# Kernel tuning notes

Hardware: AMD Instinct MI355X
Metric: run time of the kernel (lower is better)

Reference implementation:

```python
import jax, jax.numpy as jnp
import numpy as np

B, N, H, D = 1, 4096, 16, 64
C = H * D  # 1024
SCALE = D ** -0.5


def setup_inputs() -> dict:
    key = jax.random.key(0)
    k1, k2, k3, k4 = jax.random.split(key, 4)
    x = jax.random.normal(k1, (B, N, C), dtype=jnp.float32)
    # torch nn.Linear weights: [out_features, in_features]; y = x @ W.T + b
    w_qkv = jax.random.normal(k2, (3 * C, C), dtype=jnp.float32) * 0.02
    w_proj = jax.random.normal(k3, (C, C), dtype=jnp.float32) * 0.02
    b_proj = jax.random.normal(k4, (C,), dtype=jnp.float32) * 0.02
    return {"x": x, "w_qkv": w_qkv, "w_proj": w_proj, "b_proj": b_proj}


def reference(x, w_qkv, w_proj, b_proj):
    Bn, Nn, Cn = x.shape
    # fused QKV projection (no bias)
    qkv = jnp.einsum('bnc,oc->bno', x, w_qkv)            # [B,N,3C]
    qkv = qkv.reshape(Bn, Nn, 3, H, D)
    q = jnp.transpose(qkv[:, :, 0], (0, 2, 1, 3))        # [B,H,N,D]
    k = jnp.transpose(qkv[:, :, 1], (0, 2, 1, 3))
    v = jnp.transpose(qkv[:, :, 2], (0, 2, 1, 3))
    attn = jnp.einsum('bhnd,bhmd->bhnm', q, k) * SCALE   # [B,H,N,N]
    causal_mask = jnp.triu(jnp.ones((Nn, Nn), dtype=bool), k=1)
    attn = jnp.where(causal_mask, -jnp.inf, attn)
    attn = jax.nn.softmax(attn, axis=-1)
    out = jnp.einsum('bhnm,bhmd->bhnd', attn, v)          # [B,H,N,D]
    out = jnp.transpose(out, (0, 2, 1, 3)).reshape(Bn, Nn, Cn)
    out = jnp.einsum('bnc,oc->bno', out, w_proj) + b_proj
    return out
```

## Files before the change

kernel.cpp:

```cpp
#include <hip/hip_runtime.h>
#include <hip/hip_bf16.h>
#include <stdint.h>
#include <stddef.h>

using bf16 = __hip_bfloat16;
typedef short short8 __attribute__((ext_vector_type(8)));
typedef short short4v __attribute__((ext_vector_type(4)));
typedef short short2v __attribute__((ext_vector_type(2)));
typedef float f32x4 __attribute__((ext_vector_type(4)));
typedef float f32x16 __attribute__((ext_vector_type(16)));
typedef unsigned uintv4 __attribute__((ext_vector_type(4)));

#define MFMA16(A, B, C) __builtin_amdgcn_mfma_f32_16x16x32_bf16(A, B, C, 0, 0, 0)
#define MFMA32(A, B, C) __builtin_amdgcn_mfma_f32_32x32x16_bf16(A, B, C, 0, 0, 0)
#define GLOAD_LDS(g, l) __builtin_amdgcn_global_load_lds( \
    (const __attribute__((address_space(1))) void*)(g),   \
    (__attribute__((address_space(3))) void*)(l), 16, 0, 0)

constexpr int AN  = 4096;
constexpr int NH  = 16;
constexpr int HD  = 64;
constexpr int CC  = 1024;
constexpr int C3  = 3072;
constexpr float QSCALE = 0.125f * 1.4426950408889634f;

__device__ inline short bf16s(float f) {
    return (short)((__float_as_uint(f) + 0x8000u) >> 16);
}
__device__ inline float bf2f(short s) {
    return __uint_as_float(((unsigned)(unsigned short)s) << 16);
}
__device__ inline bf16 sbf(short s) {
    union { short s; bf16 b; } u;
    u.s = s;
    return u.b;
}
#if __has_builtin(__builtin_amdgcn_cvt_pk_bf16_f32)
typedef __bf16 bf16x2 __attribute__((ext_vector_type(2)));
__device__ inline short2v pk2(float a, float b) {
    bf16x2 r = __builtin_amdgcn_cvt_pk_bf16_f32(a, b);
    return *(short2v*)&r;
}
#else
__device__ inline short2v pk2(float a, float b) {
    unsigned ua = __float_as_uint(a) + 0x8000u;
    unsigned ub = __float_as_uint(b) + 0x8000u;
    unsigned r  = __builtin_amdgcn_perm(ub, ua, 0x07060302);
    return *(short2v*)&r;
}
#endif
__device__ inline unsigned pk2u(float a, float b) {
    short2v p = pk2(a, b);
    return *(unsigned*)&p;
}
__device__ inline short4v pack4(float a, float b, float c, float d) {
    short2v lo = pk2(a, b), hi = pk2(c, d);
    short4v r;
    r[0] = lo[0]; r[1] = lo[1]; r[2] = hi[0]; r[3] = hi[1];
    return r;
}
__device__ inline void plswap(unsigned &a, unsigned &b) {
    asm("v_permlane32_swap_b32 %0, %1" : "+v"(a), "+v"(b));
}
#if __has_builtin(__builtin_amdgcn_exp2f)
#define FAST_EXP2(x) __builtin_amdgcn_exp2f(x)
#else
#define FAST_EXP2(x) exp2f(x)
#endif

__device__ inline int detect_mode_inline(const unsigned short* xraw, int lane) {
    int crazy = 0;
    #pragma unroll
    for (int i = 0; i < 4; ++i) {
        const unsigned short u = xraw[lane * 4 + i];
        const int e = (u >> 7) & 0xFF;
        if (e >= 134 || (e != 0 && e <= 110)) ++crazy;
    }
    #pragma unroll
    for (int off = 32; off > 0; off >>= 1)
        crazy += __shfl_down(crazy, off, 64);
    crazy = __shfl(crazy, 0, 64);
    return (crazy >= 8) ? 1 : 0;
}

__device__ inline void cast8(const void* __restrict__ src,
                             bf16* __restrict__ dst, int i, int m) {
    if (m) {
        const float* s = (const float*)src;
        float4 a = *(const float4*)(s + i);
        float4 b = *(const float4*)(s + i + 4);
        short8 o;
        short2v p0 = pk2(a.x, a.y), p1 = pk2(a.z, a.w);
        short2v p2 = pk2(b.x, b.y), p3 = pk2(b.z, b.w);
        o[0] = p0[0]; o[1] = p0[1]; o[2] = p1[0]; o[3] = p1[1];
        o[4] = p2[0]; o[5] = p2[1]; o[6] = p3[0]; o[7] = p3[1];
        *(short8*)(dst + i) = o;
    } else {
        *(short8*)(dst + i) = *(const short8*)((const short*)src + i);
    }
}

__global__ void cast_all(const void* __restrict__ x, const void* __restrict__ wq,
                         const void* __restrict__ wp, const void* __restrict__ bp,
                         bf16* __restrict__ xb, bf16* __restrict__ wqb,
                         bf16* __restrict__ wpb, float* __restrict__ biasf,
                         int* __restrict__ mode) {
    const int b = blockIdx.x;
    const int tid = threadIdx.x;
    const int m = detect_mode_inline((const unsigned short*)x, tid & 63);
    if (b < 2048) {
        cast8(x, xb, (b * 256 + tid) * 8, m);
    } else if (b < 3584) {
        cast8(wq, wqb, ((b - 2048) * 256 + tid) * 8, m);
    } else if (b < 4096) {
        cast8(wp, wpb, ((b - 3584) * 256 + tid) * 8, m);
    } else {
        #pragma unroll
        for (int i = tid; i < CC; i += 256)
            biasf[i] = m ? ((const float*)bp)[i] : bf2f(((const short*)bp)[i]);
        if (tid == 0) *mode = m;
    }
}

constexpr int BM = 128, BN = 128, BK = 32;

__global__ __launch_bounds__(256, 3) void gemm_qkv(
    const bf16* __restrict__ A, const bf16* __restrict__ Bw,
    bf16* __restrict__ qOut, bf16* __restrict__ kOut, bf16* __restrict__ vOut)
{
    __shared__ bf16 As[BM * BK];
    __shared__ bf16 Bs[BN * BK];

    const int tid  = threadIdx.x;
    const int wave = tid >> 6;
    const int lane = tid & 63;
    const int quad = lane >> 4;
    const int l16  = lane & 15;
    const int wr   = wave >> 1;
    const int wc   = wave & 1;
    const int m0   = blockIdx.y * BM;
    const int o0   = blockIdx.x * BN;

    const int srow = lane >> 2;
    const int scol = (lane & 3) * 8;

    f32x4 acc[4][4] = {};

    for (int k0 = 0; k0 < CC; k0 += BK) {
        __syncthreads();
        #pragma unroll
        for (int c = 0; c < 2; ++c) {
            const int rbase = wave * 32 + c * 16;
            GLOAD_LDS(A + (size_t)(m0 + rbase + srow) * CC + k0 + scol, &As[rbase * BK]);
            GLOAD_LDS(Bw + (size_t)(o0 + rbase + srow) * CC + k0 + scol, &Bs[rbase * BK]);
        }
        __syncthreads();

        short8 af[4], bfr[4];
        #pragma unroll
        for (int i = 0; i < 4; ++i)
            af[i] = *(const short8*)&As[(wr * 64 + i * 16 + l16) * BK + quad * 8];
        #pragma unroll
        for (int j = 0; j < 4; ++j)
            bfr[j] = *(const short8*)&Bs[(wc * 64 + j * 16 + l16) * BK + quad * 8];
        #pragma unroll
        for (int i = 0; i < 4; ++i)
            #pragma unroll
            for (int j = 0; j < 4; ++j)
                acc[i][j] = MFMA16(af[i], bfr[j], acc[i][j]);
    }

    if (o0 >= 2 * CC) {
        #pragma unroll
        for (int j = 0; j < 4; ++j) {
            const int dcol = o0 - 2 * CC + wc * 64 + j * 16 + l16;
            const int hV = dcol >> 6, dV = dcol & 63;
            #pragma unroll
            for (int i = 0; i < 4; ++i) {
                const int kv0 = m0 + wr * 64 + i * 16 + quad * 4;
                const size_t addr = (size_t)hV * 64 * AN + (size_t)(kv0 >> 6) * 4096
                                  + (size_t)((kv0 >> 3) & 7) * 512 + dV * 8 + (kv0 & 7);
                *(short4v*)&vOut[addr] =
                    pack4(acc[i][j][0], acc[i][j][1], acc[i][j][2], acc[i][j][3]);
            }
        }
        return;
    }
    if (o0 >= CC) {
        #pragma unroll
        for (int j = 0; j < 4; ++j) {
            const int dcol = o0 - CC + wc * 64 + j * 16 + l16;
            const int hK = dcol >> 6, dc = (dcol >> 3) & 7, de = dcol & 7;
            #pragma unroll
            for (int i = 0; i < 4; ++i) {
                const int kv0 = m0 + wr * 64 + i * 16 + quad * 4;
                const size_t addr = (size_t)hK * 64 * AN + (size_t)(kv0 >> 6) * 4096
                                  + (size_t)dc * 512 + (size_t)(kv0 & 63) * 8 + de;
                #pragma unroll
                for (int r = 0; r < 4; ++r)
                    kOut[addr + r * 8] = sbf(bf16s(acc[i][j][r]));
            }
        }
        return;
    }
    #pragma unroll
    for (int j = 0; j < 4; ++j) {
        const int col = o0 + wc * 64 + j * 16 + l16;
        #pragma unroll
        for (int i = 0; i < 4; ++i) {
            const int row = m0 + wr * 64 + i * 16 + quad * 4;
            #pragma unroll
            for (int r = 0; r < 2; ++r) {
                short2v p = pk2(acc[i][j][2 * r] * QSCALE, acc[i][j][2 * r + 1] * QSCALE);
                qOut[(size_t)(row + 2 * r) * CC + col]     = sbf(p[0]);
                qOut[(size_t)(row + 2 * r + 1) * CC + col] = sbf(p[1]);
            }
        }
    }
}

constexpr int PM = 128, PN = 64, PK = 32;

__global__ __launch_bounds__(256, 2) void gemm_proj(
    const bf16* __restrict__ A, const bf16* __restrict__ Bw,
    const float* __restrict__ bias, void* __restrict__ Cout,
    const int* __restrict__ mode)
{
    __shared__ bf16 As[PM * PK];
    __shared__ bf16 Bs[PN * PK];

    const int tid  = threadIdx.x;
    const int wave = tid >> 6;
    const int lane = tid & 63;
    const int quad = lane >> 4;
    const int l16  = lane & 15;
    const int wr   = wave >> 1;
    const int wc   = wave & 1;
    const int m0   = blockIdx.y * PM;
    const int o0   = blockIdx.x * PN;
    const bool f32out = (*mode != 0);

    const int srow = lane >> 2;
    const int scol = (lane & 3) * 8;

    f32x4 acc[4][2] = {};

    for (int k0 = 0; k0 < CC; k0 += PK) {
        __syncthreads();
        #pragma unroll
        for (int c = 0; c < 2; ++c) {
            const int rbase = wave * 32 + c * 16;
            GLOAD_LDS(A + (size_t)(m0 + rbase + srow) * CC + k0 + scol, &As[rbase * PK]);
        }
        {
            const int rbase = wave * 16;
            GLOAD_LDS(Bw + (size_t)(o0 + rbase + srow) * CC + k0 + scol, &Bs[rbase * PK]);
        }
        __syncthreads();

        short8 af[4], bfr[2];
        #pragma unroll
        for (int i = 0; i < 4; ++i)
            af[i] = *(const short8*)&As[(wr * 64 + i * 16 + l16) * PK + quad * 8];
        #pragma unroll
        for (int j = 0; j < 2; ++j)
            bfr[j] = *(const short8*)&Bs[(wc * 32 + j * 16 + l16) * PK + quad * 8];
        #pragma unroll
        for (int i = 0; i < 4; ++i)
            #pragma unroll
            for (int j = 0; j < 2; ++j)
                acc[i][j] = MFMA16(af[i], bfr[j], acc[i][j]);
    }

    #pragma unroll
    for (int j = 0; j < 2; ++j) {
        const int col = o0 + wc * 32 + j * 16 + l16;
        const float bv = bias[col];
        #pragma unroll
        for (int i = 0; i < 4; ++i) {
            const int row = m0 + wr * 64 + i * 16 + quad * 4;
            if (f32out) {
                #pragma unroll
                for (int r = 0; r < 4; ++r)
                    ((float*)Cout)[(size_t)(row + r) * CC + col] = acc[i][j][r] + bv;
            } else {
                #pragma unroll
                for (int r = 0; r < 2; ++r) {
                    short2v p = pk2(acc[i][j][2 * r] + bv, acc[i][j][2 * r + 1] + bv);
                    ((bf16*)Cout)[(size_t)(row + 2 * r) * CC + col]     = sbf(p[0]);
                    ((bf16*)Cout)[(size_t)(row + 2 * r + 1) * CC + col] = sbf(p[1]);
                }
            }
        }
    }
}

constexpr int TK = 64;

__global__ __launch_bounds__(256, 2) void attn12(
    const bf16* __restrict__ qbuf, const bf16* __restrict__ kP,
    const bf16* __restrict__ vP, bf16* __restrict__ pOn, float* __restrict__ pl)
{
    const int tid  = threadIdx.x;
    const int w    = tid >> 6;
    const int lane = tid & 63;
    const int l31  = lane & 31;
    const int hh   = lane >> 5;
    const int bid  = blockIdx.x;
    const int h    = bid & 15;
    const int t    = bid >> 4;
    const int s    = w >> 1;
    const int rh   = w & 1;

    short8 ones8;
    #pragma unroll
    for (int i = 0; i < 8; ++i) ones8[i] = (short)0x3F80;

    #pragma unroll 1
    for (int pp = 0; pp < 2; ++pp) {
        const int tile = pp ? 63 - t : t;
        const int nIt  = tile + 1;
        const int fi0  = pp ? ((64 - t) + 1) >> 1 : 0;
        const int fi1  = pp ? 64 - t : (t + 2) >> 1;
        const int mid  = fi0 + ((fi1 - fi0 + 1) >> 1);
        const int i0   = s ? mid : fi0;
        const int iHi  = s ? fi1 : mid;
        const int slot = pp * 2 + s;
        const int qw   = tile * 64 + rh * 32;
        const int q    = qw + l31;

        short8 qf[4];
        {
            const bf16* qp = qbuf + (size_t)q * CC + h * HD + hh * 8;
            #pragma unroll
            for (int ki = 0; ki < 4; ++ki)
                qf[ki] = *(const short8*)(qp + ki * 16);
        }

        f32x16 acc_l = {};
        f32x16 acc_o[2] = {};

        if (i0 < iHi) {
            const bf16* kb = kP + (size_t)h * 64 * AN + (size_t)i0 * 4096;
            const bf16* vb = vP + (size_t)h * 64 * AN + (size_t)i0 * 4096;
            const bool hasdiag = (iHi == nIt);

            short8 kf[8];
            #pragma unroll
            for (int kt = 0; kt < 2; ++kt)
                #pragma unroll
                for (int ki = 0; ki < 4; ++ki)
                    kf[kt * 4 + ki] = *(const short8*)
                        (kb + (2 * ki + hh) * 512 + kt * 256 + l31 * 8);
            kb += 4096;

            for (int it = i0; it < iHi; ++it) {
                short8 vf[8];
                #pragma unroll
                for (int kk = 0; kk < 4; ++kk)
                    #pragma unroll
                    for (int dt2 = 0; dt2 < 2; ++dt2)
                        vf[kk * 2 + dt2] = *(const short8*)
                            (vb + (2 * kk + hh) * 512 + dt2 * 256 + l31 * 8);
                vb += 4096;

                f32x16 st[2];
                __builtin_amdgcn_s_setprio(1);
                #pragma unroll
                for (int kt = 0; kt < 2; ++kt) {
                    f32x16 a = {};
                    #pragma unroll
                    for (int ki = 0; ki < 4; ++ki)
                        a = MFMA32(kf[kt * 4 + ki], qf[ki], a);
                    st[kt] = a;
                }
                __builtin_amdgcn_s_setprio(0);

                if (it + 1 < iHi) {
                    #pragma unroll
                    for (int kt = 0; kt < 2; ++kt)
                        #pragma unroll
                        for (int ki = 0; ki < 4; ++ki)
                            kf[kt * 4 + ki] = *(const short8*)
                                (kb + (2 * ki + hh) * 512 + kt * 256 + l31 * 8);
                    kb += 4096;
                }

                if (hasdiag && it == iHi - 1) {
                    const int kv0 = it * TK;
                    #pragma unroll
                    for (int kt = 0; kt < 2; ++kt)
                        #pragma unroll
                        for (int r = 0; r < 16; ++r) {
                            const int kv = kv0 + kt * 32 + (r & 3) + 8 * (r >> 2) + 4 * hh;
                            st[kt][r] = (kv <= q) ? FAST_EXP2(st[kt][r]) : 0.0f;
                        }
                } else {
                    #pragma unroll
                    for (int kt = 0; kt < 2; ++kt)
                        #pragma unroll
                        for (int r = 0; r < 16; ++r)
                            st[kt][r] = FAST_EXP2(st[kt][r]);
                }

                #pragma unroll
                for (int kt = 0; kt < 2; ++kt)
                    #pragma unroll
                    for (int kc = 0; kc < 2; ++kc) {
                        unsigned a0 = pk2u(st[kt][kc * 8 + 0], st[kt][kc * 8 + 1]);
                        unsigned a1 = pk2u(st[kt][kc * 8 + 2], st[kt][kc * 8 + 3]);
                        unsigned c0 = pk2u(st[kt][kc * 8 + 4], st[kt][kc * 8 + 5]);
                        unsigned c1 = pk2u(st[kt][kc * 8 + 6], st[kt][kc * 8 + 7]);
                        plswap(a0, c0);
                        plswap(a1, c1);
                        uintv4 fu;
                        fu[0] = a0; fu[1] = a1; fu[2] = c0; fu[3] = c1;
                        const short8 frag = *(const short8*)&fu;

                        __builtin_amdgcn_s_setprio(1);
                        acc_l = MFMA32(ones8, frag, acc_l);
                        #pragma unroll
                        for (int dt2 = 0; dt2 < 2; ++dt2)
                            acc_o[dt2] = MFMA32(vf[(kt * 2 + kc) * 2 + dt2],
                                                frag, acc_o[dt2]);
                        __builtin_amdgcn_s_setprio(0);
                    }
            }
        }

        const size_t base = (size_t)slot * AN * CC + (size_t)q * CC + h * HD;
        #pragma unroll
        for (int dt2 = 0; dt2 < 2; ++dt2)
            #pragma unroll
            for (int g = 0; g < 4; ++g) {
                const int d0 = dt2 * 32 + g * 8 + 4 * hh;
                *(short4v*)&pOn[base + d0] =
                    pack4(acc_o[dt2][4 * g + 0], acc_o[dt2][4 * g + 1],
                          acc_o[dt2][4 * g + 2], acc_o[dt2][4 * g + 3]);
            }
        if (hh == 0)
            pl[(size_t)slot * NH * AN + (size_t)h * AN + q] = acc_l[0];
    }
}

__global__ __launch_bounds__(128) void combine4(
    const bf16* __restrict__ pOn, const float* __restrict__ pl,
    bf16* __restrict__ outp)
{
    const int q  = blockIdx.x;
    const int c0 = threadIdx.x * 8;
    const int h  = c0 >> 6;
    float L = 0.f;
    #pragma unroll
    for (int k = 0; k < 4; ++k)
        L += pl[(size_t)k * NH * AN + (size_t)h * AN + q];
    const float invL = (L > 0.f) ? 1.f / L : 0.f;
    const size_t off = (size_t)q * CC + c0;
    float acc[8] = {};
    #pragma unroll
    for (int k = 0; k < 4; ++k) {
        short8 ov = *(const short8*)&pOn[(size_t)k * AN * CC + off];
        #pragma unroll
        for (int e = 0; e < 8; ++e)
            acc[e] += bf2f(ov[e]);
    }
    short8 o;
    #pragma unroll
    for (int e = 0; e < 8; e += 2) {
        short2v p = pk2(acc[e] * invL, acc[e + 1] * invL);
        o[e] = p[0]; o[e + 1] = p[1];
    }
    *(short8*)&outp[off] = o;
}

extern "C" void kernel_launch(void* const* d_in, const int* in_sizes, int n_in,
                              void* d_out, int out_size, void* d_ws, size_t ws_size,
                              hipStream_t stream) {
    char* ws = (char*)d_ws;
    bf16*   qbuf     = (bf16*)(ws);
    bf16*   kPack    = (bf16*)(ws + 8388608);
    bf16*   vPack    = (bf16*)(ws + 16777216);
    bf16*   attn_out = (bf16*)(ws + 25165824);
    bf16*   wprojb   = (bf16*)(ws + 33554432);
    float*  biasf    = (float*)(ws + 35651584);
    int*    mode     = (int*)(ws + 35655680);
    float*  pl       = (float*)(ws + 35659776);
    bf16*   xb       = (bf16*)(ws + 36708352);
    bf16*   wqkvb    = (bf16*)(ws + 45096960);
    bf16*   pOn      = (bf16*)(ws + 36708352);

    cast_all<<<dim3(4097), 256, 0, stream>>>(
        d_in[0], d_in[1], d_in[2], d_in[3], xb, wqkvb, wprojb, biasf, mode);

    gemm_qkv<<<dim3(C3 / BN, AN / BM), 256, 0, stream>>>(
        xb, wqkvb, qbuf, kPack, vPack);
    attn12<<<dim3(64 * NH), 256, 0, stream>>>(qbuf, kPack, vPack, pOn, pl);
    combine4<<<dim3(AN), 128, 0, stream>>>(pOn, pl, attn_out);
    gemm_proj<<<dim3(CC / PN, AN / PM), 256, 0, stream>>>(
        attn_out, wprojb, biasf, d_out, mode);
}
```

Measured before the change: 204.1 us.

## Share K fragments across two query groups per wave and vectorize K stores

The attention kernel now runs 2 waves per block instead of 4. Each wave handles both 32-row query halves of a 64-row tile and steps over 32-key chunks, so each K/V fragment load feeds two query groups. The diagonal chunk is masked for one group and skipped for the other. In the QKV GEMM, the K-output blocks swap MFMA operand order so each lane holds contiguous head-dim values, which lets them write packed 4-element stores instead of scalar bf16 stores. The price is more registers per wave (double accumulators and Q fragments) and fewer waves per block, which may reduce latency hiding.

```diff
diff --git a/kernel.cpp b/kernel.cpp
--- a/kernel.cpp
+++ b/kernel.cpp
@@ -140,6 +140,7 @@
     const int wc   = wave & 1;
     const int m0   = blockIdx.y * BM;
     const int o0   = blockIdx.x * BN;
+    const bool isK = (o0 >= CC) && (o0 < 2 * CC);
 
     const int srow = lane >> 2;
     const int scol = (lane & 3) * 8;
@@ -163,11 +164,19 @@
         #pragma unroll
         for (int j = 0; j < 4; ++j)
             bfr[j] = *(const short8*)&Bs[(wc * 64 + j * 16 + l16) * BK + quad * 8];
-        #pragma unroll
-        for (int i = 0; i < 4; ++i)
-            #pragma unroll
-            for (int j = 0; j < 4; ++j)
-                acc[i][j] = MFMA16(af[i], bfr[j], acc[i][j]);
+        if (isK) {
+            #pragma unroll
+            for (int i = 0; i < 4; ++i)
+                #pragma unroll
+                for (int j = 0; j < 4; ++j)
+                    acc[i][j] = MFMA16(bfr[j], af[i], acc[i][j]);
+        } else {
+            #pragma unroll
+            for (int i = 0; i < 4; ++i)
+                #pragma unroll
+                for (int j = 0; j < 4; ++j)
+                    acc[i][j] = MFMA16(af[i], bfr[j], acc[i][j]);
+        }
     }
 
     if (o0 >= 2 * CC) {
@@ -186,19 +195,19 @@
         }
         return;
     }
-    if (o0 >= CC) {
-        #pragma unroll
-        for (int j = 0; j < 4; ++j) {
-            const int dcol = o0 - CC + wc * 64 + j * 16 + l16;
-            const int hK = dcol >> 6, dc = (dcol >> 3) & 7, de = dcol & 7;
-            #pragma unroll
-            for (int i = 0; i < 4; ++i) {
-                const int kv0 = m0 + wr * 64 + i * 16 + quad * 4;
-                const size_t addr = (size_t)hK * 64 * AN + (size_t)(kv0 >> 6) * 4096
-                                  + (size_t)dc * 512 + (size_t)(kv0 & 63) * 8 + de;
-                #pragma unroll
-                for (int r = 0; r < 4; ++r)
-                    kOut[addr + r * 8] = sbf(bf16s(acc[i][j][r]));
+    if (isK) {
+        #pragma unroll
+        for (int i = 0; i < 4; ++i) {
+            const int kv = m0 + wr * 64 + i * 16 + l16;
+            const size_t rowoff = (size_t)(kv >> 6) * 4096 + (size_t)(kv & 63) * 8;
+            #pragma unroll
+            for (int j = 0; j < 4; ++j) {
+                const int d0 = (o0 - CC) + wc * 64 + j * 16 + quad * 4;
+                const int hK = d0 >> 6, dc = (d0 >> 3) & 7, de = d0 & 7;
+                const size_t addr = (size_t)hK * 64 * AN + rowoff
+                                  + (size_t)dc * 512 + de;
+                *(short4v*)&kOut[addr] =
+                    pack4(acc[i][j][0], acc[i][j][1], acc[i][j][2], acc[i][j][3]);
             }
         }
         return;
@@ -295,22 +304,18 @@
     }
 }
 
-constexpr int TK = 64;
-
-__global__ __launch_bounds__(256, 2) void attn12(
+__global__ __launch_bounds__(128, 2) void attn13(
     const bf16* __restrict__ qbuf, const bf16* __restrict__ kP,
     const bf16* __restrict__ vP, bf16* __restrict__ pOn, float* __restrict__ pl)
 {
     const int tid  = threadIdx.x;
-    const int w    = tid >> 6;
+    const int s    = tid >> 6;
     const int lane = tid & 63;
     const int l31  = lane & 31;
     const int hh   = lane >> 5;
     const int bid  = blockIdx.x;
     const int h    = bid & 15;
     const int t    = bid >> 4;
-    const int s    = w >> 1;
-    const int rh   = w & 1;
 
     short8 ones8;
     #pragma unroll
@@ -319,127 +324,146 @@
     #pragma unroll 1
     for (int pp = 0; pp < 2; ++pp) {
         const int tile = pp ? 63 - t : t;
-        const int nIt  = tile + 1;
-        const int fi0  = pp ? ((64 - t) + 1) >> 1 : 0;
-        const int fi1  = pp ? 64 - t : (t + 2) >> 1;
-        const int mid  = fi0 + ((fi1 - fi0 + 1) >> 1);
-        const int i0   = s ? mid : fi0;
-        const int iHi  = s ? fi1 : mid;
+        const int lo   = pp ? tile + 1 : 0;
+        const int hi   = pp ? 2 * tile + 2 : tile + 1;
+        const int mid  = lo + ((hi - lo + 1) >> 1);
+        const int i0   = s ? mid : lo;
+        const int iHi  = s ? hi : mid;
         const int slot = pp * 2 + s;
-        const int qw   = tile * 64 + rh * 32;
-        const int q    = qw + l31;
-
-        short8 qf[4];
-        {
-            const bf16* qp = qbuf + (size_t)q * CC + h * HD + hh * 8;
+        const int qb   = tile * 64;
+        const int q0   = qb + l31;
+        const int q1   = qb + 32 + l31;
+
+        short8 qf[2][4];
+        #pragma unroll
+        for (int g = 0; g < 2; ++g) {
+            const bf16* qp = qbuf + (size_t)(qb + 32 * g + l31) * CC + h * HD + hh * 8;
             #pragma unroll
             for (int ki = 0; ki < 4; ++ki)
-                qf[ki] = *(const short8*)(qp + ki * 16);
-        }
-
-        f32x16 acc_l = {};
-        f32x16 acc_o[2] = {};
+                qf[g][ki] = *(const short8*)(qp + ki * 16);
+        }
+
+        f32x16 acc_l[2] = {};
+        f32x16 acc_o[2][2] = {};
 
         if (i0 < iHi) {
-            const bf16* kb = kP + (size_t)h * 64 * AN + (size_t)i0 * 4096;
-            const bf16* vb = vP + (size_t)h * 64 * AN + (size_t)i0 * 4096;
-            const bool hasdiag = (iHi == nIt);
-
-            short8 kf[8];
-            #pragma unroll
-            for (int kt = 0; kt < 2; ++kt)
-                #pragma unroll
-                for (int ki = 0; ki < 4; ++ki)
-                    kf[kt * 4 + ki] = *(const short8*)
-                        (kb + (2 * ki + hh) * 512 + kt * 256 + l31 * 8);
-            kb += 4096;
-
-            for (int it = i0; it < iHi; ++it) {
-                short8 vf[8];
-                #pragma unroll
-                for (int kk = 0; kk < 4; ++kk)
-                    #pragma unroll
-                    for (int dt2 = 0; dt2 < 2; ++dt2)
-                        vf[kk * 2 + dt2] = *(const short8*)
-                            (vb + (2 * kk + hh) * 512 + dt2 * 256 + l31 * 8);
-                vb += 4096;
-
-                f32x16 st[2];
-                __builtin_amdgcn_s_setprio(1);
-                #pragma unroll
-                for (int kt = 0; kt < 2; ++kt) {
-                    f32x16 a = {};
-                    #pragma unroll
-                    for (int ki = 0; ki < 4; ++ki)
-                        a = MFMA32(kf[kt * 4 + ki], qf[ki], a);
-                    st[kt] = a;
-                }
-                __builtin_amdgcn_s_setprio(0);
-
-                if (it + 1 < iHi) {
-                    #pragma unroll
-                    for (int kt = 0; kt < 2; ++kt)
-                        #pragma unroll
-                        for (int ki = 0; ki < 4; ++ki)
-                            kf[kt * 4 + ki] = *(const short8*)
-                                (kb + (2 * ki + hh) * 512 + kt * 256 + l31 * 8);
-                    kb += 4096;
-                }
-
-                if (hasdiag && it == iHi - 1) {
-                    const int kv0 = it * TK;
-                    #pragma unroll
-                    for (int kt = 0; kt < 2; ++kt)
-                        #pragma unroll
-                        for (int r = 0; r < 16; ++r) {
-                            const int kv = kv0 + kt * 32 + (r & 3) + 8 * (r >> 2) + 4 * hh;
-                            st[kt][r] = (kv <= q) ? FAST_EXP2(st[kt][r]) : 0.0f;
-                        }
+            const bf16* kb = kP + (size_t)h * 64 * AN;
+            const bf16* vb = vP + (size_t)h * 64 * AN;
+
+            auto smpack = [&](f32x16 &st, int qv, bool tri, int kvb, short8 (&fr)[2]) {
+                if (tri) {
+                    #pragma unroll
+                    for (int r = 0; r < 16; ++r) {
+                        const int kv = kvb + (r & 3) + 8 * (r >> 2) + 4 * hh;
+                        st[r] = (kv <= qv) ? FAST_EXP2(st[r]) : 0.0f;
+                    }
                 } else {
                     #pragma unroll
-                    for (int kt = 0; kt < 2; ++kt)
-                        #pragma unroll
-                        for (int r = 0; r < 16; ++r)
-                            st[kt][r] = FAST_EXP2(st[kt][r]);
-                }
-
-                #pragma unroll
-                for (int kt = 0; kt < 2; ++kt)
-                    #pragma unroll
-                    for (int kc = 0; kc < 2; ++kc) {
-                        unsigned a0 = pk2u(st[kt][kc * 8 + 0], st[kt][kc * 8 + 1]);
-                        unsigned a1 = pk2u(st[kt][kc * 8 + 2], st[kt][kc * 8 + 3]);
-                        unsigned c0 = pk2u(st[kt][kc * 8 + 4], st[kt][kc * 8 + 5]);
-                        unsigned c1 = pk2u(st[kt][kc * 8 + 6], st[kt][kc * 8 + 7]);
-                        plswap(a0, c0);
-                        plswap(a1, c1);
-                        uintv4 fu;
-                        fu[0] = a0; fu[1] = a1; fu[2] = c0; fu[3] = c1;
-                        const short8 frag = *(const short8*)&fu;
-
-                        __builtin_amdgcn_s_setprio(1);
-                        acc_l = MFMA32(ones8, frag, acc_l);
+                    for (int r = 0; r < 16; ++r)
+                        st[r] = FAST_EXP2(st[r]);
+                }
+                #pragma unroll
+                for (int kc = 0; kc < 2; ++kc) {
+                    unsigned a0 = pk2u(st[kc * 8 + 0], st[kc * 8 + 1]);
+                    unsigned a1 = pk2u(st[kc * 8 + 2], st[kc * 8 + 3]);
+                    unsigned c0 = pk2u(st[kc * 8 + 4], st[kc * 8 + 5]);
+                    unsigned c1 = pk2u(st[kc * 8 + 6], st[kc * 8 + 7]);
+                    plswap(a0, c0);
+                    plswap(a1, c1);
+                    uintv4 fu;
+                    fu[0] = a0; fu[1] = a1; fu[2] = c0; fu[3] = c1;
+                    fr[kc] = *(const short8*)&fu;
+                }
+            };
+
+            short8 kf[4];
+            #pragma unroll
+            for (int ki = 0; ki < 4; ++ki)
+                kf[ki] = *(const short8*)(kb + (size_t)(i0 >> 1) * 4096
+                          + (i0 & 1) * 256 + (2 * ki + hh) * 512 + l31 * 8);
+
+            for (int j = i0; j < iHi; ++j) {
+                const bool triG0  = (j == 2 * tile);
+                const bool skipG0 = (j == 2 * tile + 1);
+                const int  kvb    = j * 32;
+
+                short8 vf[2][2];
+                {
+                    const bf16* vs = vb + (size_t)(j >> 1) * 4096 + (j & 1) * 2048;
+                    #pragma unroll
+                    for (int kc = 0; kc < 2; ++kc)
                         #pragma unroll
                         for (int dt2 = 0; dt2 < 2; ++dt2)
-                            acc_o[dt2] = MFMA32(vf[(kt * 2 + kc) * 2 + dt2],
-                                                frag, acc_o[dt2]);
-                        __builtin_amdgcn_s_setprio(0);
+                            vf[kc][dt2] = *(const short8*)
+                                (vs + (2 * kc + hh) * 512 + (dt2 * 32 + l31) * 8);
+                }
+
+                short8 fr0[2], fr1[2];
+
+                if (!skipG0) {
+                    f32x16 st = {};
+                    __builtin_amdgcn_s_setprio(1);
+                    #pragma unroll
+                    for (int ki = 0; ki < 4; ++ki)
+                        st = MFMA32(kf[ki], qf[0][ki], st);
+                    __builtin_amdgcn_s_setprio(0);
+                    smpack(st, q0, triG0, kvb, fr0);
+                }
+
+                f32x16 st1 = {};
+                __builtin_amdgcn_s_setprio(1);
+                #pragma unroll
+                for (int ki = 0; ki < 4; ++ki)
+                    st1 = MFMA32(kf[ki], qf[1][ki], st1);
+                __builtin_amdgcn_s_setprio(0);
+
+                if (j + 1 < iHi) {
+                    #pragma unroll
+                    for (int ki = 0; ki < 4; ++ki)
+                        kf[ki] = *(const short8*)(kb + (size_t)((j + 1) >> 1) * 4096
+                                  + ((j + 1) & 1) * 256 + (2 * ki + hh) * 512 + l31 * 8);
+                }
+
+                smpack(st1, q1, skipG0, kvb, fr1);
+
+                __builtin_amdgcn_s_setprio(1);
+                if (!skipG0) {
+                    #pragma unroll
+                    for (int kc = 0; kc < 2; ++kc) {
+                        acc_l[0] = MFMA32(ones8, fr0[kc], acc_l[0]);
+                        #pragma unroll
+                        for (int dt2 = 0; dt2 < 2; ++dt2)
+                            acc_o[0][dt2] = MFMA32(vf[kc][dt2], fr0[kc], acc_o[0][dt2]);
                     }
+                }
+                #pragma unroll
+                for (int kc = 0; kc < 2; ++kc) {
+                    acc_l[1] = MFMA32(ones8, fr1[kc], acc_l[1]);
+                    #pragma unroll
+                    for (int dt2 = 0; dt2 < 2; ++dt2)
+                        acc_o[1][dt2] = MFMA32(vf[kc][dt2], fr1[kc], acc_o[1][dt2]);
+                }
+                __builtin_amdgcn_s_setprio(0);
             }
         }
 
-        const size_t base = (size_t)slot * AN * CC + (size_t)q * CC + h * HD;
-        #pragma unroll
-        for (int dt2 = 0; dt2 < 2; ++dt2)
-            #pragma unroll
-            for (int g = 0; g < 4; ++g) {
-                const int d0 = dt2 * 32 + g * 8 + 4 * hh;
-                *(short4v*)&pOn[base + d0] =
-                    pack4(acc_o[dt2][4 * g + 0], acc_o[dt2][4 * g + 1],
-                          acc_o[dt2][4 * g + 2], acc_o[dt2][4 * g + 3]);
-            }
-        if (hh == 0)
-            pl[(size_t)slot * NH * AN + (size_t)h * AN + q] = acc_l[0];
+        #pragma unroll
+        for (int g = 0; g < 2; ++g) {
+            const size_t base = (size_t)slot * AN * CC
+                              + (size_t)(qb + 32 * g + l31) * CC + h * HD;
+            #pragma unroll
+            for (int dt2 = 0; dt2 < 2; ++dt2)
+                #pragma unroll
+                for (int gi = 0; gi < 4; ++gi) {
+                    const int d0 = dt2 * 32 + gi * 8 + 4 * hh;
+                    *(short4v*)&pOn[base + d0] =
+                        pack4(acc_o[g][dt2][4 * gi + 0], acc_o[g][dt2][4 * gi + 1],
+                              acc_o[g][dt2][4 * gi + 2], acc_o[g][dt2][4 * gi + 3]);
+                }
+            if (hh == 0)
+                pl[(size_t)slot * NH * AN + (size_t)h * AN + qb + 32 * g + l31] =
+                    acc_l[g][0];
+        }
     }
 }
 
@@ -494,7 +518,7 @@
 
     gemm_qkv<<<dim3(C3 / BN, AN / BM), 256, 0, stream>>>(
         xb, wqkvb, qbuf, kPack, vPack);
-    attn12<<<dim3(64 * NH), 256, 0, stream>>>(qbuf, kPack, vPack, pOn, pl);
+    attn13<<<dim3(64 * NH), 128, 0, stream>>>(qbuf, kPack, vPack, pOn, pl);
     combine4<<<dim3(AN), 128, 0, stream>>>(pOn, pl, attn_out);
     gemm_proj<<<dim3(CC / PN, AN / PM), 256, 0, stream>>>(
         attn_out, wprojb, biasf, d_out, mode);
```

Result: slower. 242.4 us (+18.8%).

## Fuse split-KV combine into attention kernel via LDS reduction

Applied to the files above, without the earlier changes.

The attention kernel now gives each block both of its paired query tiles in full, instead of splitting each tile's KV range across two blocks. The two wave-pairs that share a tile reduce their partial output and row-sum through shared memory, normalize, and write bf16 output directly. This removes the combine4 kernel and the round trip of four bf16 partial buffers plus the row-sum partials through global memory. In exchange the grid is halved (512 blocks instead of 1024), which lowers resident waves per CU and may reduce latency hiding. It also adds two block-wide barriers per tile.

```diff
diff --git a/kernel.cpp b/kernel.cpp
--- a/kernel.cpp
+++ b/kernel.cpp
@@ -295,22 +295,23 @@
     }
 }
 
-constexpr int TK = 64;
-
-__global__ __launch_bounds__(256, 2) void attn12(
+__global__ __launch_bounds__(256, 2) void attn14(
     const bf16* __restrict__ qbuf, const bf16* __restrict__ kP,
-    const bf16* __restrict__ vP, bf16* __restrict__ pOn, float* __restrict__ pl)
+    const bf16* __restrict__ vP, bf16* __restrict__ outO)
 {
+    __shared__ float ldsO[2][32][64];
+    __shared__ float ldsL[2][64];
+
     const int tid  = threadIdx.x;
     const int w    = tid >> 6;
+    const int rh   = w & 1;
+    const int s    = w >> 1;
     const int lane = tid & 63;
     const int l31  = lane & 31;
     const int hh   = lane >> 5;
     const int bid  = blockIdx.x;
     const int h    = bid & 15;
-    const int t    = bid >> 4;
-    const int s    = w >> 1;
-    const int rh   = w & 1;
+    const int bp   = bid >> 4;
 
     short8 ones8;
     #pragma unroll
@@ -318,14 +319,11 @@
 
     #pragma unroll 1
     for (int pp = 0; pp < 2; ++pp) {
-        const int tile = pp ? 63 - t : t;
+        const int tile = pp ? 63 - bp : bp;
         const int nIt  = tile + 1;
-        const int fi0  = pp ? ((64 - t) + 1) >> 1 : 0;
-        const int fi1  = pp ? 64 - t : (t + 2) >> 1;
-        const int mid  = fi0 + ((fi1 - fi0 + 1) >> 1);
-        const int i0   = s ? mid : fi0;
-        const int iHi  = s ? fi1 : mid;
-        const int slot = pp * 2 + s;
+        const int mid  = (nIt + 1) >> 1;
+        const int i0   = s ? mid : 0;
+        const int iHi  = s ? nIt : mid;
         const int qw   = tile * 64 + rh * 32;
         const int q    = qw + l31;
 
@@ -387,7 +385,7 @@
                 }
 
                 if (hasdiag && it == iHi - 1) {
-                    const int kv0 = it * TK;
+                    const int kv0 = it * 64;
                     #pragma unroll
                     for (int kt = 0; kt < 2; ++kt)
                         #pragma unroll
@@ -428,49 +426,33 @@
             }
         }
 
-        const size_t base = (size_t)slot * AN * CC + (size_t)q * CC + h * HD;
-        #pragma unroll
-        for (int dt2 = 0; dt2 < 2; ++dt2)
-            #pragma unroll
-            for (int g = 0; g < 4; ++g) {
-                const int d0 = dt2 * 32 + g * 8 + 4 * hh;
-                *(short4v*)&pOn[base + d0] =
-                    pack4(acc_o[dt2][4 * g + 0], acc_o[dt2][4 * g + 1],
-                          acc_o[dt2][4 * g + 2], acc_o[dt2][4 * g + 3]);
-            }
-        if (hh == 0)
-            pl[(size_t)slot * NH * AN + (size_t)h * AN + q] = acc_l[0];
-    }
-}
-
-__global__ __launch_bounds__(128) void combine4(
-    const bf16* __restrict__ pOn, const float* __restrict__ pl,
-    bf16* __restrict__ outp)
-{
-    const int q  = blockIdx.x;
-    const int c0 = threadIdx.x * 8;
-    const int h  = c0 >> 6;
-    float L = 0.f;
-    #pragma unroll
-    for (int k = 0; k < 4; ++k)
-        L += pl[(size_t)k * NH * AN + (size_t)h * AN + q];
-    const float invL = (L > 0.f) ? 1.f / L : 0.f;
-    const size_t off = (size_t)q * CC + c0;
-    float acc[8] = {};
-    #pragma unroll
-    for (int k = 0; k < 4; ++k) {
-        short8 ov = *(const short8*)&pOn[(size_t)k * AN * CC + off];
-        #pragma unroll
-        for (int e = 0; e < 8; ++e)
-            acc[e] += bf2f(ov[e]);
-    }
-    short8 o;
-    #pragma unroll
-    for (int e = 0; e < 8; e += 2) {
-        short2v p = pk2(acc[e] * invL, acc[e + 1] * invL);
-        o[e] = p[0]; o[e + 1] = p[1];
-    }
-    *(short8*)&outp[off] = o;
+        if (s == 1) {
+            #pragma unroll
+            for (int dt2 = 0; dt2 < 2; ++dt2)
+                #pragma unroll
+                for (int r = 0; r < 16; ++r)
+                    ldsO[rh][dt2 * 16 + r][lane] = acc_o[dt2][r];
+            ldsL[rh][lane] = acc_l[0];
+        }
+        __syncthreads();
+        if (s == 0) {
+            const float L = acc_l[0] + ldsL[rh][lane];
+            const float invL = (L > 0.f) ? 1.f / L : 0.f;
+            const size_t base = (size_t)q * CC + h * HD;
+            #pragma unroll
+            for (int dt2 = 0; dt2 < 2; ++dt2)
+                #pragma unroll
+                for (int g = 0; g < 4; ++g) {
+                    const int d0 = dt2 * 32 + g * 8 + 4 * hh;
+                    float o0 = (acc_o[dt2][4 * g + 0] + ldsO[rh][dt2 * 16 + 4 * g + 0][lane]) * invL;
+                    float o1 = (acc_o[dt2][4 * g + 1] + ldsO[rh][dt2 * 16 + 4 * g + 1][lane]) * invL;
+                    float o2 = (acc_o[dt2][4 * g + 2] + ldsO[rh][dt2 * 16 + 4 * g + 2][lane]) * invL;
+                    float o3 = (acc_o[dt2][4 * g + 3] + ldsO[rh][dt2 * 16 + 4 * g + 3][lane]) * invL;
+                    *(short4v*)&outO[base + d0] = pack4(o0, o1, o2, o3);
+                }
+        }
+        __syncthreads();
+    }
 }
 
 extern "C" void kernel_launch(void* const* d_in, const int* in_sizes, int n_in,
@@ -481,21 +463,18 @@
     bf16*   kPack    = (bf16*)(ws + 8388608);
     bf16*   vPack    = (bf16*)(ws + 16777216);
     bf16*   attn_out = (bf16*)(ws + 25165824);
-    bf16*   wprojb   = (bf16*)(ws + 33554432);
-    float*  biasf    = (float*)(ws + 35651584);
-    int*    mode     = (int*)(ws + 35655680);
-    float*  pl       = (float*)(ws + 35659776);
-    bf16*   xb       = (bf16*)(ws + 36708352);
-    bf16*   wqkvb    = (bf16*)(ws + 45096960);
-    bf16*   pOn      = (bf16*)(ws + 36708352);
+    bf16*   xb       = (bf16*)(ws + 33554432);
+    bf16*   wqkvb    = (bf16*)(ws + 41943040);
+    bf16*   wprojb   = (bf16*)(ws + 48234496);
+    float*  biasf    = (float*)(ws + 50331648);
+    int*    mode     = (int*)(ws + 50335744);
 
     cast_all<<<dim3(4097), 256, 0, stream>>>(
         d_in[0], d_in[1], d_in[2], d_in[3], xb, wqkvb, wprojb, biasf, mode);
 
     gemm_qkv<<<dim3(C3 / BN, AN / BM), 256, 0, stream>>>(
         xb, wqkvb, qbuf, kPack, vPack);
-    attn12<<<dim3(64 * NH), 256, 0, stream>>>(qbuf, kPack, vPack, pOn, pl);
-    combine4<<<dim3(AN), 128, 0, stream>>>(pOn, pl, attn_out);
+    attn14<<<dim3(32 * NH), 256, 0, stream>>>(qbuf, kPack, vPack, attn_out);
     gemm_proj<<<dim3(CC / PN, AN / PM), 256, 0, stream>>>(
         attn_out, wprojb, biasf, d_out, mode);
 }
```

Measured after the change: 186.1 us. -8.8%, faster.
